# Kernel tuning notes

Measured on AMD Instinct MI355X. Metric: run time of the kernel, lower is better.

Reference implementation:

```python
import jax, jax.numpy as jnp
import numpy as np

B, L = 32, 128
NUM_LANG, NUM_WORD, NUM_POS, NUM_DEP, NUM_ENT, NUM_IOB = 5, 50000, 50, 50, 20, 4
LANG_D, WORD_D, POS_D, DEP_D, ENT_D, IOB_D = 50, 300, 50, 50, 50, 50
IN_D = LANG_D + WORD_D + POS_D + DEP_D + ENT_D + IOB_D  # 550
H = 200  # lstm_dim // 2 per direction
PAD_IDX, STOP_IDX = 0, 2


def setup_inputs() -> dict:
    key = jax.random.key(0)
    ks = jax.random.split(key, 24)
    f32 = jnp.float32
    w = lambda k, shape: jax.random.normal(k, shape, f32) * 0.05
    e = lambda k, n, d: jax.random.normal(k, (n, d), f32) * 0.1
    return {
        # word idxs in [3, NUM_WORD) so no PAD(0)/STOP(2): all sentences full length
        'lang_idxs': jax.random.randint(ks[0], (B, L), 0, NUM_LANG),
        'word_idxs': jax.random.randint(ks[1], (B, L), 3, NUM_WORD),
        'pos_idxs': jax.random.randint(ks[2], (B, L), 1, NUM_POS),
        'dep_idxs': jax.random.randint(ks[3], (B, L), 1, NUM_DEP),
        'ent_idxs': jax.random.randint(ks[4], (B, L), 1, NUM_ENT),
        'ent_iob_idxs': jax.random.randint(ks[5], (B, L), 1, NUM_IOB),
        'E_lang': e(ks[6], NUM_LANG, LANG_D),
        'E_word': e(ks[7], NUM_WORD, WORD_D),
        'E_pos': e(ks[8], NUM_POS, POS_D),
        'E_dep': e(ks[9], NUM_DEP, DEP_D),
        'E_ent': e(ks[10], NUM_ENT, ENT_D),
        'E_iob': e(ks[11], NUM_IOB, IOB_D),
        # biLSTM params, leading dim 2 = direction (0 fwd, 1 bwd); torch gate order i,f,g,o
        'Wih0': w(ks[12], (2, 4 * H, IN_D)),
        'Whh0': w(ks[13], (2, 4 * H, H)),
        'bih0': w(ks[14], (2, 4 * H)),
        'bhh0': w(ks[15], (2, 4 * H)),
        'Wih1': w(ks[16], (2, 4 * H, 2 * H)),
        'Whh1': w(ks[17], (2, 4 * H, H)),
        'bih1': w(ks[18], (2, 4 * H)),
        'bhh1': w(ks[19], (2, 4 * H)),
    }


def _lstm_dir(x, Wi, Wh, bi, bh, reverse):
    # x: (L, B, in) time-major; single direction LSTM
    xg = jnp.einsum('lbi,gi->lbg', x, Wi) + (bi + bh)  # precompute input gates

    def step(carry, xt):
        h, c = carry
        g = xt + h @ Wh.T
        i, f, gg, o = jnp.split(g, 4, axis=-1)
        c = jax.nn.sigmoid(f) * c + jax.nn.sigmoid(i) * jnp.tanh(gg)
        h = jax.nn.sigmoid(o) * jnp.tanh(c)
        return (h, c), h

    nb = x.shape[1]
    h0 = jnp.zeros((nb, Wh.shape[-1]), x.dtype)
    _, hs = jax.lax.scan(step, (h0, h0), xg, reverse=reverse)
    return hs  # (L, B, H), in original time order


def _bilstm_layer(x, Wih, Whh, bih, bhh):
    fwd = _lstm_dir(x, Wih[0], Whh[0], bih[0], bhh[0], False)
    bwd = _lstm_dir(x, Wih[1], Whh[1], bih[1], bhh[1], True)
    return jnp.concatenate([fwd, bwd], axis=-1)  # (L, B, 2H)


def reference(lang_idxs, word_idxs, pos_idxs, dep_idxs, ent_idxs, ent_iob_idxs,
              E_lang, E_word, E_pos, E_dep, E_ent, E_iob,
              Wih0, Whh0, bih0, bhh0, Wih1, Whh1, bih1, bhh1):
    mask = word_idxs != PAD_IDX            # (B, L); all True for these inputs
    sen_lens = mask.sum(1)                 # all == L, so sort/pack/pad are no-ops
    emb = jnp.concatenate([E_lang[lang_idxs], E_word[word_idxs], E_pos[pos_idxs],
                           E_dep[dep_idxs], E_ent[ent_idxs], E_iob[ent_iob_idxs]], axis=-1)
    # emb_drop disabled (eval mode)
    x = jnp.transpose(emb, (1, 0, 2))      # (L, B, IN_D)
    x = _bilstm_layer(x, Wih0, Whh0, bih0, bhh0)
    x = _bilstm_layer(x, Wih1, Whh1, bih1, bhh1)   # inter-layer dropout disabled
    h = jnp.transpose(x, (1, 0, 2))        # (B, L, 2H)
    f, bw = h[..., :H], h[..., H:]
    # pairwise span features: x[i,j] = h_i - h_j masked by triu(1) on [0, L-1)
    a, b = np.triu_indices(L - 1, 1)       # static: (L-1)(L-2)/2 spans, row-major in (a,b)
    span_f = f[:, b] - f[:, a]             # forward half: f_b - f_a
    span_b = bw[:, a + 1] - bw[:, b + 1]   # backward half: bw_{a+1} - bw_{b+1}
    x_span = jnp.concatenate([span_f, span_b], axis=-1)  # (B, 8001, 2H)
    return (x_span, sen_lens - 2)
```

## Files before the change

### kernel.cpp

```cpp
#include <hip/hip_runtime.h>
#include <hip/hip_bf16.h>
#include <hip/hip_fp16.h>


typedef unsigned short u16;
typedef unsigned int u32;
typedef short shortx8 __attribute__((ext_vector_type(8)));
typedef float floatx4 __attribute__((ext_vector_type(4)));
typedef _Float16 half2v __attribute__((ext_vector_type(2)));

#define B_ 32
#define L_ 128
#define H_ 200
#define K0P 576
#define K1P 416
#define NG 1600
#define NPAIR 8001
#define SPAN_ELEMS 102412800

__device__ __forceinline__ float bf2f(u16 v) {
  u32 u = ((u32)v) << 16;
  return __builtin_bit_cast(float, u);
}
__device__ __forceinline__ u16 f2bf(float f) {
  __hip_bfloat16 h = __float2bfloat16(f);
  return __builtin_bit_cast(u16, h);
}
__device__ __forceinline__ float loadF(const void* p, int idx, int isf32) {
  return isf32 ? ((const float*)p)[idx] : bf2f(((const u16*)p)[idx]);
}
__device__ __forceinline__ float dot2h(u32 w, u32 h, float acc) {
#if __has_builtin(__builtin_amdgcn_fdot2)
  return __builtin_amdgcn_fdot2(__builtin_bit_cast(half2v, w),
                                __builtin_bit_cast(half2v, h), acc, false);
#else
  half2v a = __builtin_bit_cast(half2v, w), b = __builtin_bit_cast(half2v, h);
  return acc + (float)a.x * (float)b.x + (float)a.y * (float)b.y;
#endif
}
__device__ __forceinline__ float sigf(float x) { return 1.f / (1.f + __expf(-x)); }
__device__ __forceinline__ float tanhff(float x) {
  x = fminf(fmaxf(x, -15.f), 15.f);
  float e = __expf(-2.f * x);
  return (1.f - e) / (1.f + e);
}


__global__ void sniff_kernel(const void* __restrict__ Ew, int* __restrict__ flag) {
  if (threadIdx.x != 0) return;
  const u16* p = (const u16*)Ew;
  int big = 0;
  for (int i = 0; i < 128; ++i) {
    int e = (p[i] >> 7) & 0xFF;
    if (e >= 0x84) big++;
  }
  *flag = (big >= 4) ? 1 : 0;
}


__global__ void pairs_kernel(int* pa, int* pb) {
  int a = threadIdx.x;
  if (a >= 126) return;
  int off = a * 126 - a * (a - 1) / 2;
  for (int b = a + 1; b <= 126; ++b) {
    pa[off] = a;
    pb[off] = b;
    ++off;
  }
}

__global__ void senlen_kernel(const int* __restrict__ word, void* __restrict__ out,
                              const int* __restrict__ flag) {
  int b = threadIdx.x;
  if (b >= B_) return;
  int cnt = 0;
  for (int l = 0; l < L_; ++l) cnt += (word[b * L_ + l] != 0);
  float v = (float)(cnt - 2);
  if (*flag) ((float*)out)[SPAN_ELEMS + b] = v;
  else ((u16*)out)[SPAN_ELEMS + b] = f2bf(v);
}

__global__ void embed_kernel(const int* __restrict__ lang, const int* __restrict__ word,
                             const int* __restrict__ pos, const int* __restrict__ dep,
                             const int* __restrict__ ent, const int* __restrict__ iob,
                             const void* __restrict__ El, const void* __restrict__ Ew,
                             const void* __restrict__ Ep, const void* __restrict__ Ed,
                             const void* __restrict__ Ee, const void* __restrict__ Ei,
                             u16* __restrict__ x0, const int* __restrict__ flag) {
  int row = blockIdx.x;
  int isf32 = *flag;
  int l = row >> 5, b = row & 31;
  int io = b * L_ + l;
  int li = lang[io], wi = word[io], pi = pos[io], di = dep[io], ei = ent[io], ii = iob[io];
  for (int c = threadIdx.x; c < K0P; c += 64) {
    float v = 0.f;
    if (c < 50) v = loadF(El, li * 50 + c, isf32);
    else if (c < 350) v = loadF(Ew, wi * 300 + (c - 50), isf32);
    else if (c < 400) v = loadF(Ep, pi * 50 + (c - 350), isf32);
    else if (c < 450) v = loadF(Ed, di * 50 + (c - 400), isf32);
    else if (c < 500) v = loadF(Ee, ei * 50 + (c - 450), isf32);
    else if (c < 550) v = loadF(Ei, ii * 50 + (c - 500), isf32);
    x0[row * K0P + c] = f2bf(v);
  }
}

__global__ void pack_kernel(const void* __restrict__ Wih0, const void* __restrict__ Whh0,
                            const void* __restrict__ bih0, const void* __restrict__ bhh0,
                            const void* __restrict__ Wih1, const void* __restrict__ Whh1,
                            const void* __restrict__ bih1, const void* __restrict__ bhh1,
                            u16* __restrict__ Wc0, u16* __restrict__ Wc1,
                            float* __restrict__ bias0, float* __restrict__ bias1,
                            u16* __restrict__ Whf, u16* __restrict__ x1,
                            const int* __restrict__ flag) {
  int idx = blockIdx.x * 256 + threadIdx.x;
  int isf32 = *flag;
  if (idx < 1600 * K0P) {
    int r = idx / K0P, c = idx - r * K0P;
    Wc0[idx] = (c < 550) ? f2bf(loadF(Wih0, r * 550 + c, isf32)) : (u16)0;
    return;
  }
  idx -= 1600 * K0P;
  if (idx < 1600 * K1P) {
    int r = idx / K1P, c = idx - r * K1P;
    Wc1[idx] = (c < 400) ? f2bf(loadF(Wih1, r * 400 + c, isf32)) : (u16)0;
    return;
  }
  idx -= 1600 * K1P;
  if (idx < 1600) { bias0[idx] = loadF(bih0, idx, isf32) + loadF(bhh0, idx, isf32); return; }
  idx -= 1600;
  if (idx < 1600) { bias1[idx] = loadF(bih1, idx, isf32) + loadF(bhh1, idx, isf32); return; }
  idx -= 1600;
  if (idx < 640000) {
    float s = (idx < 320000) ? loadF(Whh0, idx, isf32) : loadF(Whh1, idx - 320000, isf32);
    _Float16 h = (_Float16)s;
    Whf[idx] = __builtin_bit_cast(u16, h);
    return;
  }
  idx -= 640000;
  if (idx < 4096 * 16) {
    int row = idx >> 4, c = idx & 15;
    x1[row * K1P + 400 + c] = 0;
  }
}


__global__ __launch_bounds__(256) void gemm_bt(const u16* __restrict__ A, const u16* __restrict__ W,
                                               const float* __restrict__ bias, u16* __restrict__ C,
                                               int Ks) {
  __shared__ __align__(16) u16 As[64 * 40];
  __shared__ __align__(16) u16 Bs[64 * 40];
  int tid = threadIdx.x;
  int n0 = blockIdx.x * 64, m0 = blockIdx.y * 64;
  int lane = tid & 63, wv = tid >> 6, ln = lane & 15, quad = lane >> 4;
  floatx4 acc[4] = {{0.f, 0.f, 0.f, 0.f}, {0.f, 0.f, 0.f, 0.f}, {0.f, 0.f, 0.f, 0.f}, {0.f, 0.f, 0.f, 0.f}};
  int arow = tid >> 2, acs = (tid & 3) * 8;
  const u16* Ag = A + (size_t)(m0 + arow) * Ks + acs;
  const u16* Wg = W + (size_t)(n0 + arow) * Ks + acs;
  for (int k0 = 0; k0 < Ks; k0 += 32) {
    __syncthreads();
    *(uint4*)&As[arow * 40 + acs] = *(const uint4*)(Ag + k0);
    *(uint4*)&Bs[arow * 40 + acs] = *(const uint4*)(Wg + k0);
    __syncthreads();
    shortx8 af = *(const shortx8*)&As[(wv * 16 + ln) * 40 + quad * 8];
    shortx8 b0 = *(const shortx8*)&Bs[(ln) * 40 + quad * 8];
    shortx8 b1 = *(const shortx8*)&Bs[(16 + ln) * 40 + quad * 8];
    shortx8 b2 = *(const shortx8*)&Bs[(32 + ln) * 40 + quad * 8];
    shortx8 b3 = *(const shortx8*)&Bs[(48 + ln) * 40 + quad * 8];
    acc[0] = __builtin_amdgcn_mfma_f32_16x16x32_bf16(af, b0, acc[0], 0, 0, 0);
    acc[1] = __builtin_amdgcn_mfma_f32_16x16x32_bf16(af, b1, acc[1], 0, 0, 0);
    acc[2] = __builtin_amdgcn_mfma_f32_16x16x32_bf16(af, b2, acc[2], 0, 0, 0);
    acc[3] = __builtin_amdgcn_mfma_f32_16x16x32_bf16(af, b3, acc[3], 0, 0, 0);
  }
  int rbase = m0 + wv * 16 + quad * 4;
#pragma unroll
  for (int ns = 0; ns < 4; ++ns) {
    int cg = n0 + ns * 16 + ln;
    float bv = bias[cg];
#pragma unroll
    for (int r = 0; r < 4; ++r) {
      C[(size_t)(rbase + r) * NG + cg] = f2bf(acc[ns][r] + bv);
    }
  }
}


__global__ __launch_bounds__(448) void rec_kernel(const u16* __restrict__ xg, const u16* __restrict__ Whf,
                                                  int layer, u16* __restrict__ x1, float* __restrict__ hs) {
  int tid = threadIdx.x;
  int batch = blockIdx.x >> 1, dir = blockIdx.x & 1;
  __shared__ __align__(16) u16 hsh[H_];
  __shared__ float gsh[800];
  uint4 wA[25], wB[25];
  if (tid < 400) {
    const uint4* wa = (const uint4*)(Whf + (size_t)((layer * 2 + dir) * 800 + tid) * 200);
    const uint4* wb = (const uint4*)(Whf + (size_t)((layer * 2 + dir) * 800 + tid + 400) * 200);
#pragma unroll
    for (int i = 0; i < 25; ++i) { wA[i] = wa[i]; wB[i] = wb[i]; }
  }
  float cst = 0.f;
  if (tid < H_) hsh[tid] = 0;
  __syncthreads();
  for (int t = 0; t < L_; ++t) {
    int tt = dir ? (L_ - 1 - t) : t;
    if (tid < 400) {
      const u16* xgrow = xg + (size_t)(tt * B_ + batch) * NG + dir * 800;
      float a0 = bf2f(xgrow[tid]);
      float a1 = bf2f(xgrow[tid + 400]);
      const uint4* hv4 = (const uint4*)hsh;
#pragma unroll
      for (int kk = 0; kk < 25; ++kk) {
        uint4 hv = hv4[kk];
        a0 = dot2h(wA[kk].x, hv.x, a0);
        a0 = dot2h(wA[kk].y, hv.y, a0);
        a0 = dot2h(wA[kk].z, hv.z, a0);
        a0 = dot2h(wA[kk].w, hv.w, a0);
        a1 = dot2h(wB[kk].x, hv.x, a1);
        a1 = dot2h(wB[kk].y, hv.y, a1);
        a1 = dot2h(wB[kk].z, hv.z, a1);
        a1 = dot2h(wB[kk].w, hv.w, a1);
      }
      gsh[tid] = a0;
      gsh[tid + 400] = a1;
    }
    __syncthreads();
    if (tid < H_) {
      float gi = gsh[tid], gf = gsh[200 + tid], gg = gsh[400 + tid], go = gsh[600 + tid];
      cst = sigf(gf) * cst + sigf(gi) * tanhff(gg);
      float h = sigf(go) * tanhff(cst);
      _Float16 hh = (_Float16)h;
      hsh[tid] = __builtin_bit_cast(u16, hh);
      int orow = tt * B_ + batch;
      if (layer == 0) {
        x1[(size_t)orow * K1P + dir * H_ + tid] = f2bf(h);
      } else {
        hs[(size_t)orow * 400 + dir * H_ + tid] = h;
      }
    }
    __syncthreads();
  }
}


__global__ void span_kernel(const float* __restrict__ hs, const int* __restrict__ pa,
                            const int* __restrict__ pb, void* __restrict__ outp,
                            const int* __restrict__ flag) {
  int bb = blockIdx.y;
  int p0 = blockIdx.x * 16;
  int tid = threadIdx.x;
  int isf32 = *flag;
  for (int idx = tid; idx < 16 * 200; idx += 256) {
    int p = p0 + idx / 200;
    if (p >= NPAIR) return;
    int dd2 = idx - (idx / 200) * 200;
    int dd = dd2 * 2;
    int a = pa[p], b = pb[p];
    int r1 = (dd < 200) ? b : (a + 1);
    int r2 = (dd < 200) ? a : (b + 1);
    const float* h1 = hs + (size_t)(r1 * B_ + bb) * 400 + dd;
    const float* h2 = hs + (size_t)(r2 * B_ + bb) * 400 + dd;
    float v0 = h1[0] - h2[0];
    float v1 = h1[1] - h2[1];
    size_t o2 = (size_t)(bb * NPAIR + p) * 200 + dd2;
    if (isf32) {
      ((float2*)outp)[o2] = make_float2(v0, v1);
    } else {
      ((u32*)outp)[o2] = (u32)f2bf(v0) | ((u32)f2bf(v1) << 16);
    }
  }
}


extern "C" void kernel_launch(void* const* d_in, const int* in_sizes, int n_in,
                              void* d_out, int out_size, void* d_ws, size_t ws_size,
                              hipStream_t stream) {
  const int* lang = (const int*)d_in[0];
  const int* word = (const int*)d_in[1];
  const int* pos = (const int*)d_in[2];
  const int* dep = (const int*)d_in[3];
  const int* ent = (const int*)d_in[4];
  const int* iob = (const int*)d_in[5];

  char* ws = (char*)d_ws;
  int* flag = (int*)(ws + 0);
  int* pa = (int*)(ws + 4096);
  int* pb = (int*)(ws + 36864);
  u16* x0 = (u16*)(ws + 69632);
  u16* Wc0 = (u16*)(ws + 4788224);
  u16* Wc1 = (u16*)(ws + 6631424);
  float* bias0 = (float*)(ws + 7962624);
  float* bias1 = (float*)(ws + 7969024);
  u16* Whf = (u16*)(ws + 7975424);
  u16* x1 = (u16*)(ws + 9255424);
  float* hs1 = (float*)(ws + 12663296);
  u16* xg = (u16*)(ws + 19216896);

  hipLaunchKernelGGL(sniff_kernel, dim3(1), dim3(64), 0, stream, d_in[7], flag);
  hipLaunchKernelGGL(pairs_kernel, dim3(1), dim3(128), 0, stream, pa, pb);
  hipLaunchKernelGGL(senlen_kernel, dim3(1), dim3(64), 0, stream, word, d_out, flag);
  hipLaunchKernelGGL(embed_kernel, dim3(4096), dim3(64), 0, stream,
                     lang, word, pos, dep, ent, iob,
                     d_in[6], d_in[7], d_in[8], d_in[9], d_in[10], d_in[11], x0, flag);
  hipLaunchKernelGGL(pack_kernel, dim3(8969), dim3(256), 0, stream,
                     d_in[12], d_in[13], d_in[14], d_in[15],
                     d_in[16], d_in[17], d_in[18], d_in[19],
                     Wc0, Wc1, bias0, bias1, Whf, x1, flag);
  hipLaunchKernelGGL(gemm_bt, dim3(25, 64), dim3(256), 0, stream, x0, Wc0, bias0, xg, K0P);
  hipLaunchKernelGGL(rec_kernel, dim3(64), dim3(448), 0, stream, xg, Whf, 0, x1, hs1);
  hipLaunchKernelGGL(gemm_bt, dim3(25, 64), dim3(256), 0, stream, x1, Wc1, bias1, xg, K1P);
  hipLaunchKernelGGL(rec_kernel, dim3(64), dim3(448), 0, stream, xg, Whf, 1, x1, hs1);
  hipLaunchKernelGGL(span_kernel, dim3(501, 32), dim3(256), 0, stream, hs1, pa, pb, d_out, flag);
}
```

Baseline: 1.018 ms.

## Prefetch next-step gate inputs in recurrence, widen span stores, merge prep kernels

The recurrent kernel now loads the next timestep's precomputed input gates before the current step's dot products, which takes global-load latency off the serial path. It also splits the recurrent dot product into two independent accumulator chains to add ILP, and raises the launch-bounds minimum to 2 blocks. The span kernel now handles 8 elements per thread with float4 loads and 128-bit stores over 64 pairs per block, cutting instruction count and memory transactions on the dominant output write. Three tiny setup kernels are merged into one to save launch overhead.

```diff
diff --git a/kernel.cpp b/kernel.cpp
--- a/kernel.cpp
+++ b/kernel.cpp
@@ -46,39 +46,42 @@
 }
 
 
-__global__ void sniff_kernel(const void* __restrict__ Ew, int* __restrict__ flag) {
-  if (threadIdx.x != 0) return;
-  const u16* p = (const u16*)Ew;
-  int big = 0;
-  for (int i = 0; i < 128; ++i) {
-    int e = (p[i] >> 7) & 0xFF;
-    if (e >= 0x84) big++;
-  }
-  *flag = (big >= 4) ? 1 : 0;
-}
-
-
-__global__ void pairs_kernel(int* pa, int* pb) {
-  int a = threadIdx.x;
-  if (a >= 126) return;
-  int off = a * 126 - a * (a - 1) / 2;
-  for (int b = a + 1; b <= 126; ++b) {
-    pa[off] = a;
-    pb[off] = b;
-    ++off;
-  }
-}
-
-__global__ void senlen_kernel(const int* __restrict__ word, void* __restrict__ out,
-                              const int* __restrict__ flag) {
-  int b = threadIdx.x;
-  if (b >= B_) return;
-  int cnt = 0;
-  for (int l = 0; l < L_; ++l) cnt += (word[b * L_ + l] != 0);
-  float v = (float)(cnt - 2);
-  if (*flag) ((float*)out)[SPAN_ELEMS + b] = v;
-  else ((u16*)out)[SPAN_ELEMS + b] = f2bf(v);
-}
+__global__ void prep_kernel(const void* __restrict__ Ew, const int* __restrict__ word,
+                            int* __restrict__ flag, int* __restrict__ pa, int* __restrict__ pb,
+                            void* __restrict__ out) {
+  __shared__ int sflag;
+  int tid = threadIdx.x;
+  if (tid == 0) {
+    const u16* p = (const u16*)Ew;
+    int big = 0;
+    for (int i = 0; i < 128; ++i) {
+      int e = (p[i] >> 7) & 0xFF;
+      if (e >= 0x84) big++;
+    }
+    int f = (big >= 4) ? 1 : 0;
+    *flag = f;
+    sflag = f;
+  }
+  if (tid < 126) {
+    int a = tid;
+    int off = a * 126 - a * (a - 1) / 2;
+    for (int b = a + 1; b <= 126; ++b) {
+      pa[off] = a;
+      pb[off] = b;
+      ++off;
+    }
+  }
+  __syncthreads();
+  if (tid >= 128 && tid < 128 + B_) {
+    int b = tid - 128;
+    int cnt = 0;
+    for (int l = 0; l < L_; ++l) cnt += (word[b * L_ + l] != 0);
+    float v = (float)(cnt - 2);
+    if (sflag) ((float*)out)[SPAN_ELEMS + b] = v;
+    else ((u16*)out)[SPAN_ELEMS + b] = f2bf(v);
+  }
+}
+
 
 __global__ void embed_kernel(const int* __restrict__ lang, const int* __restrict__ word,
                              const int* __restrict__ pos, const int* __restrict__ dep,
@@ -103,6 +106,7 @@
     x0[row * K0P + c] = f2bf(v);
   }
 }
+
 
 __global__ void pack_kernel(const void* __restrict__ Wih0, const void* __restrict__ Whh0,
                             const void* __restrict__ bih0, const void* __restrict__ bhh0,
@@ -184,8 +188,8 @@
 }
 
 
-__global__ __launch_bounds__(448) void rec_kernel(const u16* __restrict__ xg, const u16* __restrict__ Whf,
-                                                  int layer, u16* __restrict__ x1, float* __restrict__ hs) {
+__global__ __launch_bounds__(448, 2) void rec_kernel(const u16* __restrict__ xg, const u16* __restrict__ Whf,
+                                                     int layer, u16* __restrict__ x1, float* __restrict__ hs) {
   int tid = threadIdx.x;
   int batch = blockIdx.x >> 1, dir = blockIdx.x & 1;
   __shared__ __align__(16) u16 hsh[H_];
@@ -199,16 +203,24 @@
   }
   float cst = 0.f;
   if (tid < H_) hsh[tid] = 0;
+  int rstep = (dir ? -B_ : B_) * NG;
+  const u16* xr = xg + (size_t)((dir ? (L_ - 1) * B_ : 0) + batch) * NG + dir * 800;
+  float a0 = 0.f, a1 = 0.f;
+  if (tid < 400) { a0 = bf2f(xr[tid]); a1 = bf2f(xr[tid + 400]); }
   __syncthreads();
   for (int t = 0; t < L_; ++t) {
     int tt = dir ? (L_ - 1 - t) : t;
+    float n0 = 0.f, n1 = 0.f;
     if (tid < 400) {
-      const u16* xgrow = xg + (size_t)(tt * B_ + batch) * NG + dir * 800;
-      float a0 = bf2f(xgrow[tid]);
-      float a1 = bf2f(xgrow[tid + 400]);
+      if (t + 1 < L_) {
+        const u16* xn = xr + (ptrdiff_t)(t + 1) * rstep;
+        n0 = bf2f(xn[tid]);
+        n1 = bf2f(xn[tid + 400]);
+      }
+      float c0 = 0.f, c1 = 0.f;
       const uint4* hv4 = (const uint4*)hsh;
 #pragma unroll
-      for (int kk = 0; kk < 25; ++kk) {
+      for (int kk = 0; kk < 25; kk += 2) {
         uint4 hv = hv4[kk];
         a0 = dot2h(wA[kk].x, hv.x, a0);
         a0 = dot2h(wA[kk].y, hv.y, a0);
@@ -218,9 +230,20 @@
         a1 = dot2h(wB[kk].y, hv.y, a1);
         a1 = dot2h(wB[kk].z, hv.z, a1);
         a1 = dot2h(wB[kk].w, hv.w, a1);
+        if (kk + 1 < 25) {
+          uint4 hw = hv4[kk + 1];
+          c0 = dot2h(wA[kk + 1].x, hw.x, c0);
+          c0 = dot2h(wA[kk + 1].y, hw.y, c0);
+          c0 = dot2h(wA[kk + 1].z, hw.z, c0);
+          c0 = dot2h(wA[kk + 1].w, hw.w, c0);
+          c1 = dot2h(wB[kk + 1].x, hw.x, c1);
+          c1 = dot2h(wB[kk + 1].y, hw.y, c1);
+          c1 = dot2h(wB[kk + 1].z, hw.z, c1);
+          c1 = dot2h(wB[kk + 1].w, hw.w, c1);
+        }
       }
-      gsh[tid] = a0;
-      gsh[tid + 400] = a1;
+      gsh[tid] = a0 + c0;
+      gsh[tid + 400] = a1 + c1;
     }
     __syncthreads();
     if (tid < H_) {
@@ -236,35 +259,44 @@
         hs[(size_t)orow * 400 + dir * H_ + tid] = h;
       }
     }
+    a0 = n0;
+    a1 = n1;
     __syncthreads();
   }
 }
 
 
-__global__ void span_kernel(const float* __restrict__ hs, const int* __restrict__ pa,
-                            const int* __restrict__ pb, void* __restrict__ outp,
-                            const int* __restrict__ flag) {
+__global__ __launch_bounds__(256) void span_kernel(const float* __restrict__ hs, const int* __restrict__ pa,
+                                                   const int* __restrict__ pb, void* __restrict__ outp,
+                                                   const int* __restrict__ flag) {
   int bb = blockIdx.y;
-  int p0 = blockIdx.x * 16;
-  int tid = threadIdx.x;
+  int p0 = blockIdx.x * 64;
   int isf32 = *flag;
-  for (int idx = tid; idx < 16 * 200; idx += 256) {
-    int p = p0 + idx / 200;
-    if (p >= NPAIR) return;
-    int dd2 = idx - (idx / 200) * 200;
-    int dd = dd2 * 2;
+  for (int idx = threadIdx.x; idx < 64 * 50; idx += 256) {
+    int pr = idx / 50;
+    int q = idx - pr * 50;
+    int p = p0 + pr;
+    if (p >= NPAIR) continue;
     int a = pa[p], b = pb[p];
-    int r1 = (dd < 200) ? b : (a + 1);
-    int r2 = (dd < 200) ? a : (b + 1);
-    const float* h1 = hs + (size_t)(r1 * B_ + bb) * 400 + dd;
-    const float* h2 = hs + (size_t)(r2 * B_ + bb) * 400 + dd;
-    float v0 = h1[0] - h2[0];
-    float v1 = h1[1] - h2[1];
-    size_t o2 = (size_t)(bb * NPAIR + p) * 200 + dd2;
+    int fwd = (q < 25);
+    int r1 = fwd ? b : (a + 1);
+    int r2 = fwd ? a : (b + 1);
+    int col = q * 8;
+    const float4* h1 = (const float4*)(hs + (size_t)(r1 * B_ + bb) * 400 + col);
+    const float4* h2 = (const float4*)(hs + (size_t)(r2 * B_ + bb) * 400 + col);
+    float4 x0 = h1[0], x1v = h1[1], y0 = h2[0], y1 = h2[1];
+    float4 d0 = make_float4(x0.x - y0.x, x0.y - y0.y, x0.z - y0.z, x0.w - y0.w);
+    float4 d1 = make_float4(x1v.x - y1.x, x1v.y - y1.y, x1v.z - y1.z, x1v.w - y1.w);
     if (isf32) {
-      ((float2*)outp)[o2] = make_float2(v0, v1);
+      float4* o = (float4*)outp + (size_t)(bb * NPAIR + p) * 100 + q * 2;
+      o[0] = d0;
+      o[1] = d1;
     } else {
-      ((u32*)outp)[o2] = (u32)f2bf(v0) | ((u32)f2bf(v1) << 16);
+      u32 w0 = (u32)f2bf(d0.x) | ((u32)f2bf(d0.y) << 16);
+      u32 w1 = (u32)f2bf(d0.z) | ((u32)f2bf(d0.w) << 16);
+      u32 w2 = (u32)f2bf(d1.x) | ((u32)f2bf(d1.y) << 16);
+      u32 w3 = (u32)f2bf(d1.z) | ((u32)f2bf(d1.w) << 16);
+      ((uint4*)outp)[(size_t)(bb * NPAIR + p) * 50 + q] = make_uint4(w0, w1, w2, w3);
     }
   }
 }
@@ -294,9 +326,7 @@
   float* hs1 = (float*)(ws + 12663296);
   u16* xg = (u16*)(ws + 19216896);
 
-  hipLaunchKernelGGL(sniff_kernel, dim3(1), dim3(64), 0, stream, d_in[7], flag);
-  hipLaunchKernelGGL(pairs_kernel, dim3(1), dim3(128), 0, stream, pa, pb);
-  hipLaunchKernelGGL(senlen_kernel, dim3(1), dim3(64), 0, stream, word, d_out, flag);
+  hipLaunchKernelGGL(prep_kernel, dim3(1), dim3(256), 0, stream, d_in[7], word, flag, pa, pb, d_out);
   hipLaunchKernelGGL(embed_kernel, dim3(4096), dim3(64), 0, stream,
                      lang, word, pos, dep, ent, iob,
                      d_in[6], d_in[7], d_in[8], d_in[9], d_in[10], d_in[11], x0, flag);
@@ -308,5 +338,5 @@
   hipLaunchKernelGGL(rec_kernel, dim3(64), dim3(448), 0, stream, xg, Whf, 0, x1, hs1);
   hipLaunchKernelGGL(gemm_bt, dim3(25, 64), dim3(256), 0, stream, x1, Wc1, bias1, xg, K1P);
   hipLaunchKernelGGL(rec_kernel, dim3(64), dim3(448), 0, stream, xg, Whf, 1, x1, hs1);
-  hipLaunchKernelGGL(span_kernel, dim3(501, 32), dim3(256), 0, stream, hs1, pa, pb, d_out, flag);
-}
+  hipLaunchKernelGGL(span_kernel, dim3(126, 32), dim3(256), 0, stream, hs1, pa, pb, d_out, flag);
+}
```

After: 964.1 us. 1.06x faster.
